# Optimization experiments

Hardware: AMD Instinct MI355X
Metric: run time of the kernel (lower is better)

The kernel has to match this reference:

```python
import jax, jax.numpy as jnp
import numpy as np

N_NODES = 100000
N_EDGE_PAIRS = 800000  # undirected pairs -> 1.6M directed edges
DIM_IN = 128
NUM_CLASSES = 16
N_ITERS = 5


def _log_normalize(a):
    return a - jax.nn.logsumexp(a, axis=-1, keepdims=True)


def setup_inputs() -> dict:
    key = jax.random.key(0)
    k1, k2, k3, k4, k5 = jax.random.split(key, 5)
    # reciprocal directed edges: edges 2i and 2i+1 are reverses of each other
    src = jax.random.randint(k1, (N_EDGE_PAIRS,), 0, N_NODES)
    dst = jax.random.randint(k2, (N_EDGE_PAIRS,), 0, N_NODES)
    e_src = jnp.stack([src, dst], axis=1).reshape(-1)  # [E]
    e_dst = jnp.stack([dst, src], axis=1).reshape(-1)  # [E]
    edge_index = jnp.stack([e_src, e_dst], axis=0)     # [2, E]
    E = e_src.shape[0]
    rv = jnp.arange(E).reshape(-1, 2)[:, ::-1].reshape(-1)  # reverse-edge permutation
    x = jax.random.normal(k3, (N_NODES, DIM_IN), dtype=jnp.float32)
    W = jax.random.normal(k4, (DIM_IN, NUM_CLASSES), dtype=jnp.float32) * 0.1
    b = jnp.zeros((NUM_CLASSES,), dtype=jnp.float32)
    dim_param = NUM_CLASSES * (NUM_CLASSES + 1) // 2
    param = jax.random.normal(k5, (dim_param,), dtype=jnp.float32) * 0.1
    return {"x": x, "W": W, "b": b, "param": param,
            "edge_index": edge_index, "rv": rv}


def reference(x, W, b, param, edge_index, rv):
    N = x.shape[0]
    C = W.shape[1]
    # MLP (num_hidden=0 -> single Linear) + LogSoftmax
    log_b0 = jax.nn.log_softmax(x @ W + b, axis=-1)  # [N, C]
    # coupling matrix logH (symmetric), detached since learn_coupling=False
    rid, cid = np.tril_indices(C)
    logT = jnp.zeros((C, C), dtype=x.dtype).at[rid, cid].set(
        jax.nn.log_sigmoid(param * 10.0))
    logH = logT + jnp.triu(logT.T, 1)
    logH = jax.lax.stop_gradient(logH)
    src, dst = edge_index[0], edge_index[1]
    E = src.shape[0]
    log_msg = jnp.full((E, C), -float(np.log(C)), dtype=x.dtype)
    log_b = log_b0
    for _ in range(N_ITERS):
        # message: gather beliefs at source, subtract reverse message
        t = log_b[src] - log_msg[rv]                                    # [E, C]
        raw = jax.nn.logsumexp(t[:, :, None] + logH[None, :, :], axis=1)  # [E, C]
        log_msg = _log_normalize(raw)
        # aggregate (scatter-add) into destination nodes, then update
        agg = jax.ops.segment_sum(log_msg, dst, num_segments=N)         # [N, C]
        log_b = _log_normalize(agg + log_b0)
    return log_b
```

## Files before the change

kernel.cpp:

```cpp
#include <hip/hip_runtime.h>
#include <hip/hip_fp16.h>
#include <math.h>

#define NN      100000
#define EE      1600000
#define DIN     128
#define CC      16
#define NITERS  5
#define NBLKS   100000
#define UU      5
#define GRID_E  (NBLKS / (UU * 4))
#define NEGLOGC (-2.772588722239781f)
#define QS      128.0f
#define QINV    (1.0f / 128.0f)
#define QCLAMP  8.0f
#define GRID_U  782

#if __has_builtin(__builtin_amdgcn_mfma_f32_16x16x16bf16_1k)
#define USE_1K 1
#else
#define USE_1K 0
#endif

typedef float f4  __attribute__((ext_vector_type(4)));
typedef float v4f __attribute__((ext_vector_type(4)));
typedef short v4s __attribute__((ext_vector_type(4)));
typedef unsigned short u8h __attribute__((ext_vector_type(8)));
typedef unsigned long long ull;

__device__ __forceinline__ unsigned short f2h(float f) {
    return __half_as_ushort(__float2half(f));
}
__device__ __forceinline__ float h2f(unsigned short u) {
    return __half2float(__ushort_as_half(u));
}
__device__ __forceinline__ unsigned int pack_h(float lo, float hi) {
    return (unsigned int)f2h(lo) | ((unsigned int)f2h(hi) << 16);
}
__device__ __forceinline__ unsigned short f2bf(float f) {
    unsigned int u = __float_as_uint(f);
    unsigned int r = u + 0x7fffu + ((u >> 16) & 1u);
    return (unsigned short)(r >> 16);
}

__global__ __launch_bounds__(256) void k_setup(
    const float* __restrict__ x, const float* __restrict__ W,
    const float* __restrict__ b, const float* __restrict__ param,
    float* __restrict__ M, float* __restrict__ logb0,
    unsigned short* __restrict__ agg16)
{
    __shared__ float WT[CC][132];

    {
        f4 w0 = *(const f4*)(W + threadIdx.x * 8);
        f4 w1 = *(const f4*)(W + threadIdx.x * 8 + 4);
#pragma unroll
        for (int i = 0; i < 4; ++i) {
            int idx = threadIdx.x * 8 + i;
            WT[idx & 15][idx >> 4] = w0[i];
        }
#pragma unroll
        for (int i = 0; i < 4; ++i) {
            int idx = threadIdx.x * 8 + 4 + i;
            WT[idx & 15][idx >> 4] = w1[i];
        }
    }

    if (blockIdx.x == 0 && threadIdx.x < CC * (CC + 1) / 2) {
        int i = threadIdx.x;
        int r = 0;
        while ((r + 1) * (r + 2) / 2 <= i) ++r;
        int c = i - r * (r + 1) / 2;
        float z = param[i] * 10.0f;
        float s = 1.0f / (1.0f + __expf(-z));
        M[r * CC + c] = s;
        if (r != c) M[c * CC + r] = s;
    }

    __syncthreads();

    if (blockIdx.x == 0 && threadIdx.x < CC) {
        float s = 0.f;
        for (int c = 0; c < CC; ++c) s += M[threadIdx.x * CC + c];
        M[256 + threadIdx.x] = s;
    }

    int idx = blockIdx.x * 256 + threadIdx.x;
    agg16[idx] = 0;

    int node = idx >> 4;
    int cls  = idx & 15;
    const f4* xr4 = (const f4*)(x + (long)node * DIN);
    const f4* wr4 = (const f4*)(&WT[cls][0]);
    float acc = b[cls];
#pragma unroll 8
    for (int k4 = 0; k4 < DIN / 4; ++k4) {
        f4 xv = __builtin_nontemporal_load(xr4 + k4);
        f4 wv = wr4[k4];
        acc = fmaf(xv.x, wv.x, acc);
        acc = fmaf(xv.y, wv.y, acc);
        acc = fmaf(xv.z, wv.z, acc);
        acc = fmaf(xv.w, wv.w, acc);
    }
    float m = acc;
    for (int off = 8; off; off >>= 1) m = fmaxf(m, __shfl_xor(m, off, 16));
    float s = __expf(acc - m);
    for (int off = 8; off; off >>= 1) s += __shfl_xor(s, off, 16);
    logb0[idx] = acc - m - __logf(s);
}

template <bool RD_MSG, bool WR_MSG>
__global__ __launch_bounds__(256) void k_edges_s(
    const int* __restrict__ esrc, const float* __restrict__ logb,
    const float* __restrict__ Mg, ull* __restrict__ agg4,
    ull* __restrict__ msg8)
{
    const int lane = threadIdx.x & 63;
    const int wid  = blockIdx.x * 4 + (threadIdx.x >> 6);
    const int m    = lane & 15;
    const int q    = lane >> 4;

    const int ed = lane >> 2;
    const int j4 = lane & 3;
    const int sl = (j4 << 4) | ed;

#if USE_1K
    v4s mfrag;
#pragma unroll
    for (int jj = 0; jj < 4; ++jj)
        mfrag[jj] = (short)f2bf(Mg[m * CC + 4 * q + jj]);
#endif
    f4 rs = *(const f4*)(Mg + 256 + 4 * q);

    int srcv[UU];
    ull mw[UU];
#pragma unroll
    for (int u = 0; u < UU; ++u) {
        const long blk = (long)wid * UU + u;
        srcv[u] = __builtin_nontemporal_load(esrc + blk * 16 + m);
        if (RD_MSG)
            mw[u] = __builtin_nontemporal_load(msg8 + blk * 64 + q * 16 + (m ^ 1));
    }
    f4 lb[UU];
#pragma unroll
    for (int u = 0; u < UU; ++u)
        lb[u] = *(const f4*)(logb + (long)srcv[u] * CC + 4 * q);

#pragma unroll
    for (int u = 0; u < UU; ++u) {
        const long blk = (long)wid * UU + u;

        float mv0 = 0.f, mv1 = 0.f, mv2 = 0.f, mv3 = 0.f;
        if (RD_MSG) {
            mv0 = h2f((unsigned short)(mw[u] & 0xffffu));
            mv1 = h2f((unsigned short)((mw[u] >> 16) & 0xffffu));
            mv2 = h2f((unsigned short)((mw[u] >> 32) & 0xffffu));
            mv3 = h2f((unsigned short)(mw[u] >> 48));
        }

        float e0 = __expf(lb[u].x - mv0);
        float e1f = __expf(lb[u].y - mv1);
        float e2 = __expf(lb[u].z - mv2);
        float e3 = __expf(lb[u].w - mv3);

        float Tm = e0 * rs.x;
        Tm = fmaf(e1f, rs.y, Tm);
        Tm = fmaf(e2, rs.z, Tm);
        Tm = fmaf(e3, rs.w, Tm);
        Tm += __shfl_xor(Tm, 16, 64);
        Tm += __shfl_xor(Tm, 32, 64);
        float lT = __logf(Tm);

        float D0, D1, D2, D3;
#if USE_1K
        v4s a;
        a[0] = (short)f2bf(e0); a[1] = (short)f2bf(e1f);
        a[2] = (short)f2bf(e2); a[3] = (short)f2bf(e3);
        v4f acc = {0.f, 0.f, 0.f, 0.f};
        v4f D = __builtin_amdgcn_mfma_f32_16x16x16bf16_1k(mfrag, a, acc, 0, 0, 0);
        D0 = D[0]; D1 = D[1]; D2 = D[2]; D3 = D[3];
#else
        float ee[4] = {e0, e1f, e2, e3};
        float g1[4], g2[4], g3[4];
#pragma unroll
        for (int jj = 0; jj < 4; ++jj) {
            g1[jj] = __shfl_xor(ee[jj], 16, 64);
            g2[jj] = __shfl_xor(ee[jj], 32, 64);
            g3[jj] = __shfl_xor(ee[jj], 48, 64);
        }
        float Dv[4];
#pragma unroll
        for (int i = 0; i < 4; ++i) {
            const float* Mr = Mg + (4 * q + i) * CC;
            float d = 0.f;
#pragma unroll
            for (int jj = 0; jj < 4; ++jj) {
                d = fmaf(Mr[4 * q + jj],       ee[jj], d);
                d = fmaf(Mr[4 * (q ^ 1) + jj], g1[jj], d);
                d = fmaf(Mr[4 * (q ^ 2) + jj], g2[jj], d);
                d = fmaf(Mr[4 * (q ^ 3) + jj], g3[jj], d);
            }
            Dv[i] = d;
        }
        D0 = Dv[0]; D1 = Dv[1]; D2 = Dv[2]; D3 = Dv[3];
#endif
        float n0 = __logf(D0) - lT;
        float n1 = __logf(D1) - lT;
        float n2 = __logf(D2) - lT;
        float n3 = __logf(D3) - lT;

        if (WR_MSG) {
            ull w = (ull)pack_h(n0, n1) | ((ull)pack_h(n2, n3) << 32);
            __builtin_nontemporal_store(w, msg8 + blk * 64 + q * 16 + m);
        }

        int dstv = __shfl_xor(srcv[u], 1, 16);

        unsigned int q0 = (unsigned int)(fminf(fmaxf(-n0, 0.f), QCLAMP) * QS + 0.5f);
        unsigned int q1 = (unsigned int)(fminf(fmaxf(-n1, 0.f), QCLAMP) * QS + 0.5f);
        unsigned int q2 = (unsigned int)(fminf(fmaxf(-n2, 0.f), QCLAMP) * QS + 0.5f);
        unsigned int q3 = (unsigned int)(fminf(fmaxf(-n3, 0.f), QCLAMP) * QS + 0.5f);
        ull p = (ull)q0 | ((ull)q1 << 16) | ((ull)q2 << 32) | ((ull)q3 << 48);

        ull v = __shfl(p, sl, 64);
        int d = __shfl(dstv, ed, 16);
        atomicAdd(&agg4[(long)d * 4 + j4], v);
    }
}

__global__ __launch_bounds__(256) void k_update(
    const float* __restrict__ logb0, unsigned short* __restrict__ agg16,
    float* __restrict__ out)
{
    const int t = blockIdx.x * 256 + threadIdx.x;
    const long base = (long)t * 8;
    if (base >= (long)NN * CC) return;

    u8h av = *(const u8h*)(agg16 + base);
    *(u8h*)(agg16 + base) = (u8h){0,0,0,0,0,0,0,0};

    f4 l0 = *(const f4*)(logb0 + base);
    f4 l1 = *(const f4*)(logb0 + base + 4);

    float v[8];
#pragma unroll
    for (int i = 0; i < 4; ++i) {
        v[i]     = fmaf(-(float)av[i],     QINV, l0[i]);
        v[4 + i] = fmaf(-(float)av[4 + i], QINV, l1[i]);
    }
    float mx = v[0];
#pragma unroll
    for (int i = 1; i < 8; ++i) mx = fmaxf(mx, v[i]);
    mx = fmaxf(mx, __shfl_xor(mx, 1, 64));

    float s = 0.f;
#pragma unroll
    for (int i = 0; i < 8; ++i) s += __expf(v[i] - mx);
    s += __shfl_xor(s, 1, 64);
    float lz = mx + __logf(s);

    f4 o0, o1;
#pragma unroll
    for (int i = 0; i < 4; ++i) { o0[i] = v[i] - lz; o1[i] = v[4 + i] - lz; }
    *(f4*)(out + base)     = o0;
    *(f4*)(out + base + 4) = o1;
}

extern "C" void kernel_launch(void* const* d_in, const int* in_sizes, int n_in,
                              void* d_out, int out_size, void* d_ws, size_t ws_size,
                              hipStream_t stream)
{
    const float* x     = (const float*)d_in[0];
    const float* W     = (const float*)d_in[1];
    const float* b     = (const float*)d_in[2];
    const float* param = (const float*)d_in[3];
    const int*   eidx  = (const int*)d_in[4];
    const int*   esrc  = eidx;

    char* ws = (char*)d_ws;
    float* M     = (float*)ws;
    float* logb0 = (float*)(ws + 4096);
    float* logb  = (float*)(ws + 4096 + 6400000);
    unsigned short* agg16 = (unsigned short*)(ws + 12804096);
    ull*   agg4  = (ull*)agg16;
    ull*   msg8  = (ull*)(ws + 16004096);
    float* outp  = (float*)d_out;

    k_setup<<<NN * CC / 256, 256, 0, stream>>>(x, W, b, param, M, logb0, agg16);

    const float* curb = logb0;
    for (int it = 0; it < NITERS; ++it) {
        if (it == 0)
            k_edges_s<false, true><<<GRID_E, 256, 0, stream>>>(
                esrc, curb, M, agg4, msg8);
        else if (it == NITERS - 1)
            k_edges_s<true, false><<<GRID_E, 256, 0, stream>>>(
                esrc, curb, M, agg4, msg8);
        else
            k_edges_s<true, true><<<GRID_E, 256, 0, stream>>>(
                esrc, curb, M, agg4, msg8);
        float* dst = (it == NITERS - 1) ? outp : logb;
        k_update<<<GRID_U, 256, 0, stream>>>(logb0, agg16, dst);
        curb = dst;
    }
}
```

Measured before the change: 542.3 us.

## Interleave node beliefs and fp16 aggregates into one 128-byte row per node

Merges the per-node belief array and the quantized aggregation buffer into one interleaved row per node: 64 bytes of beliefs followed by 32 bytes of accumulators, padded to 128 bytes. The aim is for the gather of source beliefs and the atomic scatter to a node to touch the same cache line, improving locality for random node accesses. The update kernel reads and clears the aggregate from the row and writes the new belief back in place. In exchange the working-set stride grows and some bytes per row are padding, and reads and atomics now hit the same lines within one kernel.

New measurement: 613.3 us. +13.1%, slower.

```diff
diff --git a/kernel.cpp b/kernel.cpp
--- a/kernel.cpp
+++ b/kernel.cpp
@@ -16,6 +16,12 @@
 #define QCLAMP  8.0f
 #define GRID_U  782
 
+#define ROWF    32
+#define ROWH    64
+#define AGGH    32
+#define ROWU    16
+#define AGGU    8
+
 #if __has_builtin(__builtin_amdgcn_mfma_f32_16x16x16bf16_1k)
 #define USE_1K 1
 #else
@@ -47,7 +53,7 @@
     const float* __restrict__ x, const float* __restrict__ W,
     const float* __restrict__ b, const float* __restrict__ param,
     float* __restrict__ M, float* __restrict__ logb0,
-    unsigned short* __restrict__ agg16)
+    float* __restrict__ st)
 {
     __shared__ float WT[CC][132];
 
@@ -86,10 +92,11 @@
     }
 
     int idx = blockIdx.x * 256 + threadIdx.x;
-    agg16[idx] = 0;
-
     int node = idx >> 4;
     int cls  = idx & 15;
+
+    ((unsigned short*)st)[(long)node * ROWH + AGGH + cls] = 0;
+
     const f4* xr4 = (const f4*)(x + (long)node * DIN);
     const f4* wr4 = (const f4*)(&WT[cls][0]);
     float acc = b[cls];
@@ -106,20 +113,23 @@
     for (int off = 8; off; off >>= 1) m = fmaxf(m, __shfl_xor(m, off, 16));
     float s = __expf(acc - m);
     for (int off = 8; off; off >>= 1) s += __shfl_xor(s, off, 16);
-    logb0[idx] = acc - m - __logf(s);
+    float lb = acc - m - __logf(s);
+    logb0[idx] = lb;
+    st[(long)node * ROWF + cls] = lb;
 }
 
 template <bool RD_MSG, bool WR_MSG>
 __global__ __launch_bounds__(256) void k_edges_s(
-    const int* __restrict__ esrc, const float* __restrict__ logb,
-    const float* __restrict__ Mg, ull* __restrict__ agg4,
-    ull* __restrict__ msg8)
+    const int* __restrict__ esrc, const float* __restrict__ st,
+    const float* __restrict__ Mg, ull* __restrict__ msg8)
 {
     const int lane = threadIdx.x & 63;
     const int wid  = blockIdx.x * 4 + (threadIdx.x >> 6);
     const int m    = lane & 15;
     const int q    = lane >> 4;
 
+    ull* stw = (ull*)st;
+
     const int ed = lane >> 2;
     const int j4 = lane & 3;
     const int sl = (j4 << 4) | ed;
@@ -144,7 +154,7 @@
     f4 lb[UU];
 #pragma unroll
     for (int u = 0; u < UU; ++u)
-        lb[u] = *(const f4*)(logb + (long)srcv[u] * CC + 4 * q);
+        lb[u] = *(const f4*)(st + (long)srcv[u] * ROWF + 4 * q);
 
 #pragma unroll
     for (int u = 0; u < UU; ++u) {
@@ -224,23 +234,28 @@
 
         ull v = __shfl(p, sl, 64);
         int d = __shfl(dstv, ed, 16);
-        atomicAdd(&agg4[(long)d * 4 + j4], v);
-    }
-}
-
+        atomicAdd(&stw[(long)d * ROWU + AGGU + j4], v);
+    }
+}
+
+template <bool FINAL>
 __global__ __launch_bounds__(256) void k_update(
-    const float* __restrict__ logb0, unsigned short* __restrict__ agg16,
+    const float* __restrict__ logb0, float* __restrict__ st,
     float* __restrict__ out)
 {
     const int t = blockIdx.x * 256 + threadIdx.x;
-    const long base = (long)t * 8;
-    if (base >= (long)NN * CC) return;
-
-    u8h av = *(const u8h*)(agg16 + base);
-    *(u8h*)(agg16 + base) = (u8h){0,0,0,0,0,0,0,0};
-
-    f4 l0 = *(const f4*)(logb0 + base);
-    f4 l1 = *(const f4*)(logb0 + base + 4);
+    if (t >= 2 * NN) return;
+    const int node = t >> 1;
+    const int h    = t & 1;
+
+    unsigned short* agg16 = (unsigned short*)st;
+    const long ab = (long)node * ROWH + AGGH + h * 8;
+    u8h av = *(const u8h*)(agg16 + ab);
+    *(u8h*)(agg16 + ab) = (u8h){0,0,0,0,0,0,0,0};
+
+    const long db = (long)node * CC + h * 8;
+    f4 l0 = *(const f4*)(logb0 + db);
+    f4 l1 = *(const f4*)(logb0 + db + 4);
 
     float v[8];
 #pragma unroll
@@ -262,8 +277,14 @@
     f4 o0, o1;
 #pragma unroll
     for (int i = 0; i < 4; ++i) { o0[i] = v[i] - lz; o1[i] = v[4 + i] - lz; }
-    *(f4*)(out + base)     = o0;
-    *(f4*)(out + base + 4) = o1;
+    if (FINAL) {
+        *(f4*)(out + db)     = o0;
+        *(f4*)(out + db + 4) = o1;
+    } else {
+        float* bp = st + (long)node * ROWF + h * 8;
+        *(f4*)(bp)     = o0;
+        *(f4*)(bp + 4) = o1;
+    }
 }
 
 extern "C" void kernel_launch(void* const* d_in, const int* in_sizes, int n_in,
@@ -279,28 +300,26 @@
 
     char* ws = (char*)d_ws;
     float* M     = (float*)ws;
-    float* logb0 = (float*)(ws + 4096);
-    float* logb  = (float*)(ws + 4096 + 6400000);
-    unsigned short* agg16 = (unsigned short*)(ws + 12804096);
-    ull*   agg4  = (ull*)agg16;
-    ull*   msg8  = (ull*)(ws + 16004096);
+    float* st    = (float*)(ws + 4096);
+    float* logb0 = (float*)(ws + 4096 + 12800000);
+    ull*   msg8  = (ull*)(ws + 4096 + 12800000 + 6400000);
     float* outp  = (float*)d_out;
 
-    k_setup<<<NN * CC / 256, 256, 0, stream>>>(x, W, b, param, M, logb0, agg16);
-
-    const float* curb = logb0;
+    k_setup<<<NN * CC / 256, 256, 0, stream>>>(x, W, b, param, M, logb0, st);
+
     for (int it = 0; it < NITERS; ++it) {
         if (it == 0)
             k_edges_s<false, true><<<GRID_E, 256, 0, stream>>>(
-                esrc, curb, M, agg4, msg8);
+                esrc, st, M, msg8);
         else if (it == NITERS - 1)
             k_edges_s<true, false><<<GRID_E, 256, 0, stream>>>(
-                esrc, curb, M, agg4, msg8);
+                esrc, st, M, msg8);
         else
             k_edges_s<true, true><<<GRID_E, 256, 0, stream>>>(
-                esrc, curb, M, agg4, msg8);
-        float* dst = (it == NITERS - 1) ? outp : logb;
-        k_update<<<GRID_U, 256, 0, stream>>>(logb0, agg16, dst);
-        curb = dst;
-    }
-}
+                esrc, st, M, msg8);
+        if (it == NITERS - 1)
+            k_update<true><<<GRID_U, 256, 0, stream>>>(logb0, st, outp);
+        else
+            k_update<false><<<GRID_U, 256, 0, stream>>>(logb0, st, outp);
+    }
+}
```
